# Kernel optimization log

Hardware: AMD Instinct MI355X
Metric: run time of the kernel (lower is better)

## Reference

```python
import jax, jax.numpy as jnp
import numpy as np

TOP_K = 2
SCALING = 32.0 / 16.0  # alpha / rank


def setup_inputs() -> dict:
    key = jax.random.key(0)
    ks = jax.random.split(key, 8)
    B_, S, D = 4, 4096, 2048
    E, R, H = 5, 16, 256
    return {
        "x": jax.random.normal(ks[0], (B_, S, D), jnp.float32),
        "base_output": jax.random.normal(ks[1], (B_, S, D), jnp.float32),
        "A": jax.random.normal(ks[2], (E, D, R), jnp.float32) * (1.0 / R),
        "B": jax.random.normal(ks[3], (E, R, D), jnp.float32) * 0.02,
        "W1": jax.random.normal(ks[4], (D, H), jnp.float32) * (1.0 / np.sqrt(D)),
        "b1": jnp.zeros((H,), jnp.float32),
        "W2": jax.random.normal(ks[5], (H, E), jnp.float32) * (1.0 / np.sqrt(H)),
        "b2": jnp.zeros((E,), jnp.float32),
    }


def reference(x, base_output, A, B, W1, b1, W2, b2):
    # Router: Linear -> SiLU -> Linear -> softmax
    routing_logits = jax.nn.silu(x @ W1 + b1) @ W2 + b2          # [B,S,E]
    routing_weights = jax.nn.softmax(routing_logits, axis=-1)
    top_k_weights, top_k_indices = jax.lax.top_k(routing_weights, TOP_K)  # [B,S,K]
    top_k_weights = top_k_weights / top_k_weights.sum(-1, keepdims=True)

    # Dense per-expert LoRA eval (faithful to original): x @ A_e @ B_e * scaling
    low = jnp.einsum('bsd,edr->bser', x, A)                       # [B,S,E,R]
    expert_outputs = jnp.einsum('bser,erd->bsed', low, B) * SCALING  # [B,S,E,D]

    # Gather selected experts and combine with normalized weights
    gathered = jnp.take_along_axis(expert_outputs, top_k_indices[..., None], axis=2)  # [B,S,K,D]
    combined = (gathered * top_k_weights[..., None]).sum(axis=2)  # [B,S,D]
    return base_output + combined
```

## Files before the change

kernel.cpp:

```cpp
#include <hip/hip_runtime.h>
#include <math.h>

#define N_TOK 16384
#define D_DIM 2048
#define H_DIM 256
#define E_NUM 5
#define R_DIM 16
#define ER 80

#define NCT 21
#define KG_N 64

typedef _Float16 half8 __attribute__((ext_vector_type(8)));
typedef float f32x4 __attribute__((ext_vector_type(4)));

__global__ __launch_bounds__(256) void pack_w_kernel(
    const float* __restrict__ W1, const float* __restrict__ A,
    _Float16* __restrict__ Whi, _Float16* __restrict__ Wlo) {
  const int idx = blockIdx.x * 256 + threadIdx.x;
  const int lane = idx & 63;
  const int kgct = idx >> 6;
  const int kg = kgct & 63;
  const int ct = kgct >> 6;
  const int k0 = kg * 32 + ((lane >> 4) << 3);
  const int par = lane & 15;
  float v[8];
  if (ct < 16) {
    const int col = ct * 16 + par;
#pragma unroll
    for (int j = 0; j < 8; ++j) v[j] = W1[(size_t)(k0 + j) * H_DIM + col];
  } else {
    const float* Ae = A + (size_t)(ct - 16) * D_DIM * R_DIM;
#pragma unroll
    for (int j = 0; j < 8; ++j) v[j] = Ae[(size_t)(k0 + j) * R_DIM + par];
  }
  half8 hv, lv;
#pragma unroll
  for (int j = 0; j < 8; ++j) {
    const _Float16 hh = (_Float16)v[j];
    hv[j] = hh;
    lv[j] = (_Float16)(v[j] - (float)hh);
  }
  ((half8*)Whi)[(size_t)kgct * 64 + lane] = hv;
  ((half8*)Wlo)[(size_t)kgct * 64 + lane] = lv;
}

__global__ __launch_bounds__(256, 3) void xgemm_kernel(
    const float* __restrict__ x, const float* __restrict__ b1,
    const _Float16* __restrict__ Whi, const _Float16* __restrict__ Wlo,
    const float* __restrict__ W2, float* __restrict__ plog,
    float* __restrict__ P) {
  __shared__ _Float16 lds[2][2][4][64][8];
  __shared__ float w2s[H_DIM * E_NUM];
  __shared__ float plbuf[4][64][E_NUM];
  const int t = threadIdx.x;
  const int tok0 = blockIdx.x * 64;
  const int y = blockIdx.y;
  const int lane = t & 63;
  const int w = t >> 6;
  const int sr = t >> 2;
  const int sq = t & 3;
  const int lq = lane >> 4;
  const int lp = lane & 15;

  const float* xrow = x + (size_t)(tok0 + sr) * D_DIM + (sq << 3);

  {
    float xv[8];
    *(float4*)&xv[0] = *(const float4*)(xrow);
    *(float4*)&xv[4] = *(const float4*)(xrow + 4);
    half8 hv, lv;
#pragma unroll
    for (int j = 0; j < 8; ++j) {
      const _Float16 hh = (_Float16)xv[j];
      hv[j] = hh;
      lv[j] = (_Float16)(xv[j] - (float)hh);
    }
    *(half8*)&lds[0][0][sq][sr ^ sq][0] = hv;
    *(half8*)&lds[0][1][sq][sr ^ sq][0] = lv;
  }

  const half8* WH = (const half8*)Whi;
  const half8* WL = (const half8*)Wlo;

  if (y < 2) {
    f32x4 acc[4][2];
#pragma unroll
    for (int i = 0; i < 4; ++i)
#pragma unroll
      for (int j = 0; j < 2; ++j) acc[i][j] = (f32x4)0.f;
    const int ctg0 = (y << 3) + (w << 1);
    int cur = 0;
    for (int kg = 0; kg < KG_N; ++kg) {
      __syncthreads();
      const bool more = (kg < KG_N - 1);
      float xv[8];
      if (more) {
        const float* src = xrow + (kg + 1) * 32;
        *(float4*)&xv[0] = *(const float4*)(src);
        *(float4*)&xv[4] = *(const float4*)(src + 4);
      }
      half8 bh[2], bl[2];
#pragma unroll
      for (int ct = 0; ct < 2; ++ct) {
        const size_t wo = ((size_t)(ctg0 + ct) * 64 + kg) * 64 + lane;
        bh[ct] = WH[wo];
        bl[ct] = WL[wo];
      }
#pragma unroll
      for (int rt = 0; rt < 4; ++rt) {
        const int r = ((rt << 4) + lp) ^ lq;
        const half8 ah = *(const half8*)&lds[cur][0][lq][r][0];
        const half8 al = *(const half8*)&lds[cur][1][lq][r][0];
#pragma unroll
        for (int ct = 0; ct < 2; ++ct) {
          acc[rt][ct] = __builtin_amdgcn_mfma_f32_16x16x32_f16(al, bh[ct], acc[rt][ct], 0, 0, 0);
          acc[rt][ct] = __builtin_amdgcn_mfma_f32_16x16x32_f16(ah, bl[ct], acc[rt][ct], 0, 0, 0);
          acc[rt][ct] = __builtin_amdgcn_mfma_f32_16x16x32_f16(ah, bh[ct], acc[rt][ct], 0, 0, 0);
        }
      }
      if (more) {
        half8 hv, lv;
#pragma unroll
        for (int j = 0; j < 8; ++j) {
          const _Float16 hh = (_Float16)xv[j];
          hv[j] = hh;
          lv[j] = (_Float16)(xv[j] - (float)hh);
        }
        *(half8*)&lds[cur ^ 1][0][sq][sr ^ sq][0] = hv;
        *(half8*)&lds[cur ^ 1][1][sq][sr ^ sq][0] = lv;
      }
      cur ^= 1;
    }

    for (int i = t; i < H_DIM * E_NUM; i += 256) w2s[i] = W2[i];
    __syncthreads();
    const int colb = (y << 7) + (w << 5);
#pragma unroll
    for (int rt = 0; rt < 4; ++rt) {
      float pl[4][5];
#pragma unroll
      for (int rg = 0; rg < 4; ++rg)
#pragma unroll
        for (int e = 0; e < 5; ++e) pl[rg][e] = 0.f;
#pragma unroll
      for (int ct = 0; ct < 2; ++ct) {
        const int col = colb + (ct << 4) + lp;
        const float bb = b1[col];
        float w2c[5];
#pragma unroll
        for (int e = 0; e < 5; ++e) w2c[e] = w2s[col * 5 + e];
#pragma unroll
        for (int rg = 0; rg < 4; ++rg) {
          float v = acc[rt][ct][rg] + bb;
          v = v / (1.f + expf(-v));
#pragma unroll
          for (int e = 0; e < 5; ++e) pl[rg][e] = fmaf(v, w2c[e], pl[rg][e]);
        }
      }
#pragma unroll
      for (int m = 1; m < 16; m <<= 1)
#pragma unroll
        for (int rg = 0; rg < 4; ++rg)
#pragma unroll
          for (int e = 0; e < 5; ++e) pl[rg][e] += __shfl_xor(pl[rg][e], m, 64);
      if (lp == 0) {
        const int rl0 = (rt << 4) + (lq << 2);
#pragma unroll
        for (int rg = 0; rg < 4; ++rg)
#pragma unroll
          for (int e = 0; e < 5; ++e) plbuf[w][rl0 + rg][e] = pl[rg][e];
      }
    }
    __syncthreads();
    for (int i = t; i < 64 * E_NUM; i += 256) {
      const int row = i / E_NUM;
      const int e = i - row * E_NUM;
      const float s = plbuf[0][row][e] + plbuf[1][row][e] +
                      plbuf[2][row][e] + plbuf[3][row][e];
      plog[((size_t)y * N_TOK + tok0 + row) * E_NUM + e] = s;
    }
  } else {
    f32x4 acc[5];
#pragma unroll
    for (int j = 0; j < 5; ++j) acc[j] = (f32x4)0.f;
    int cur = 0;
    for (int kg = 0; kg < KG_N; ++kg) {
      __syncthreads();
      const bool more = (kg < KG_N - 1);
      float xv[8];
      if (more) {
        const float* src = xrow + (kg + 1) * 32;
        *(float4*)&xv[0] = *(const float4*)(src);
        *(float4*)&xv[4] = *(const float4*)(src + 4);
      }
      half8 bh[5], bl[5];
#pragma unroll
      for (int ct = 0; ct < 5; ++ct) {
        const size_t wo = ((size_t)(16 + ct) * 64 + kg) * 64 + lane;
        bh[ct] = WH[wo];
        bl[ct] = WL[wo];
      }
      {
        const int r = ((w << 4) + lp) ^ lq;
        const half8 ah = *(const half8*)&lds[cur][0][lq][r][0];
        const half8 al = *(const half8*)&lds[cur][1][lq][r][0];
#pragma unroll
        for (int ct = 0; ct < 5; ++ct) {
          acc[ct] = __builtin_amdgcn_mfma_f32_16x16x32_f16(al, bh[ct], acc[ct], 0, 0, 0);
          acc[ct] = __builtin_amdgcn_mfma_f32_16x16x32_f16(ah, bl[ct], acc[ct], 0, 0, 0);
          acc[ct] = __builtin_amdgcn_mfma_f32_16x16x32_f16(ah, bh[ct], acc[ct], 0, 0, 0);
        }
      }
      if (more) {
        half8 hv, lv;
#pragma unroll
        for (int j = 0; j < 8; ++j) {
          const _Float16 hh = (_Float16)xv[j];
          hv[j] = hh;
          lv[j] = (_Float16)(xv[j] - (float)hh);
        }
        *(half8*)&lds[cur ^ 1][0][sq][sr ^ sq][0] = hv;
        *(half8*)&lds[cur ^ 1][1][sq][sr ^ sq][0] = lv;
      }
      cur ^= 1;
    }
#pragma unroll
    for (int ct = 0; ct < 5; ++ct)
#pragma unroll
      for (int rg = 0; rg < 4; ++rg) {
        const int row = tok0 + (w << 4) + (lq << 2) + rg;
        P[(size_t)row * ER + (ct << 4) + lp] = acc[ct][rg];
      }
  }
}

__global__ __launch_bounds__(256, 4) void combine_kernel(
    const float* __restrict__ P, const float* __restrict__ Bm,
    const float* __restrict__ base, const float* __restrict__ plog,
    const float* __restrict__ b2, float* __restrict__ out) {
  __shared__ float Pl[32][80];
  __shared__ float sc[32][5];
  const int t = threadIdx.x;
  const int wg = __builtin_amdgcn_readfirstlane(t >> 6);
  const int c4 = ((blockIdx.x & 7) << 8) + ((t & 63) << 2);
  const int tokb = (blockIdx.x >> 3) << 5;
  const int r0 = wg << 3;

  if (t < 32) {
    const float* p0 = plog + (size_t)(tokb + t) * E_NUM;
    const float* p1 = plog + ((size_t)N_TOK + tokb + t) * E_NUM;
    float lg[5];
#pragma unroll
    for (int e = 0; e < 5; ++e) lg[e] = p0[e] + p1[e] + b2[e];
    int e0 = 0;
#pragma unroll
    for (int e = 1; e < 5; ++e) if (lg[e] > lg[e0]) e0 = e;
    int e1 = (e0 == 0) ? 1 : 0;
#pragma unroll
    for (int e = 0; e < 5; ++e) if (e != e0 && lg[e] > lg[e1]) e1 = e;
    const float qq = expf(lg[e1] - lg[e0]);
    const float s0 = 2.f / (1.f + qq);
    const float s1 = qq * s0;
#pragma unroll
    for (int e = 0; e < 5; ++e)
      sc[t][e] = (e == e0) ? s0 : ((e == e1) ? s1 : 0.f);
  }
  __syncthreads();
  for (int idx = t; idx < 640; idx += 256) {
    const int row = idx / 20;
    const int off = (idx % 20) << 2;
    float4 v = *(const float4*)(P + (size_t)(tokb + row) * ER + off);
    v.x *= sc[row][(off + 0) >> 4];
    v.y *= sc[row][(off + 1) >> 4];
    v.z *= sc[row][(off + 2) >> 4];
    v.w *= sc[row][(off + 3) >> 4];
    *(float4*)&Pl[row][off] = v;
  }
  __syncthreads();

  float4 acc[8];
#pragma unroll
  for (int i = 0; i < 8; ++i) acc[i] = make_float4(0.f, 0.f, 0.f, 0.f);

  float4 bmA[4], bmB[4];
#pragma unroll
  for (int r = 0; r < 4; ++r)
    bmA[r] = *(const float4*)(Bm + (size_t)r * D_DIM + c4);

  for (int k0 = 0; k0 < ER; k0 += 8) {
#pragma unroll
    for (int r = 0; r < 4; ++r)
      bmB[r] = *(const float4*)(Bm + (size_t)(k0 + 4 + r) * D_DIM + c4);
#pragma unroll
    for (int i = 0; i < 8; ++i) {
      float pv[4];
      *(float4*)pv = *(const float4*)&Pl[r0 + i][k0];
      acc[i].x = fmaf(pv[0], bmA[0].x, fmaf(pv[1], bmA[1].x, fmaf(pv[2], bmA[2].x, fmaf(pv[3], bmA[3].x, acc[i].x))));
      acc[i].y = fmaf(pv[0], bmA[0].y, fmaf(pv[1], bmA[1].y, fmaf(pv[2], bmA[2].y, fmaf(pv[3], bmA[3].y, acc[i].y))));
      acc[i].z = fmaf(pv[0], bmA[0].z, fmaf(pv[1], bmA[1].z, fmaf(pv[2], bmA[2].z, fmaf(pv[3], bmA[3].z, acc[i].z))));
      acc[i].w = fmaf(pv[0], bmA[0].w, fmaf(pv[1], bmA[1].w, fmaf(pv[2], bmA[2].w, fmaf(pv[3], bmA[3].w, acc[i].w))));
    }
    if (k0 + 8 < ER) {
#pragma unroll
      for (int r = 0; r < 4; ++r)
        bmA[r] = *(const float4*)(Bm + (size_t)(k0 + 8 + r) * D_DIM + c4);
    }
#pragma unroll
    for (int i = 0; i < 8; ++i) {
      float pv[4];
      *(float4*)pv = *(const float4*)&Pl[r0 + i][k0 + 4];
      acc[i].x = fmaf(pv[0], bmB[0].x, fmaf(pv[1], bmB[1].x, fmaf(pv[2], bmB[2].x, fmaf(pv[3], bmB[3].x, acc[i].x))));
      acc[i].y = fmaf(pv[0], bmB[0].y, fmaf(pv[1], bmB[1].y, fmaf(pv[2], bmB[2].y, fmaf(pv[3], bmB[3].y, acc[i].y))));
      acc[i].z = fmaf(pv[0], bmB[0].z, fmaf(pv[1], bmB[1].z, fmaf(pv[2], bmB[2].z, fmaf(pv[3], bmB[3].z, acc[i].z))));
      acc[i].w = fmaf(pv[0], bmB[0].w, fmaf(pv[1], bmB[1].w, fmaf(pv[2], bmB[2].w, fmaf(pv[3], bmB[3].w, acc[i].w))));
    }
  }

#pragma unroll
  for (int i = 0; i < 8; ++i) {
    const size_t o = (size_t)(tokb + r0 + i) * D_DIM + c4;
    const float4 b = *(const float4*)(base + o);
    float4 r;
    r.x = acc[i].x + b.x;
    r.y = acc[i].y + b.y;
    r.z = acc[i].z + b.z;
    r.w = acc[i].w + b.w;
    *(float4*)(out + o) = r;
  }
}

extern "C" void kernel_launch(void* const* d_in, const int* in_sizes, int n_in,
                              void* d_out, int out_size, void* d_ws,
                              size_t ws_size, hipStream_t stream) {
  const float* x  = (const float*)d_in[0];
  const float* bo = (const float*)d_in[1];
  const float* A  = (const float*)d_in[2];
  const float* Bm = (const float*)d_in[3];
  const float* W1 = (const float*)d_in[4];
  const float* b1 = (const float*)d_in[5];
  const float* W2 = (const float*)d_in[6];
  const float* b2 = (const float*)d_in[7];
  float* out = (float*)d_out;

  char* ws = (char*)d_ws;
  float* P = (float*)ws;
  _Float16* Whi = (_Float16*)(ws + 5242880);
  _Float16* Wlo = (_Float16*)(ws + 5242880 + 1376256);
  float* plog = (float*)(ws + 5242880 + 2 * 1376256);

  pack_w_kernel<<<336, 256, 0, stream>>>(W1, A, Whi, Wlo);
  xgemm_kernel<<<dim3(N_TOK / 64, 3), 256, 0, stream>>>(x, b1, Whi, Wlo, W2,
                                                        plog, P);
  combine_kernel<<<(N_TOK / 32) * (D_DIM / 256), 256, 0, stream>>>(
      P, Bm, bo, plog, b2, out);
}
```

Baseline: 442.0 us.

## Use single-fp16 MFMA for LoRA projections and combine, prefetch router weights

The LoRA down-projection in xgemm drops the hi/lo split and runs one fp16 MFMA per tile instead of three. The combine GEMM now uses fp16 MFMA with B pre-packed into fragment layout, replacing the scalar fp32 FMA loop. The router GEMM is unrolled by two so the next k-step's weight fragments are prefetched into registers. The aim is less MFMA and VALU work in the LoRA path and more overlap of weight loads, at the cost of reduced precision in the expert outputs and a scattered scalar store pattern for the output.

Result: faster. 386.5 us (-12.6%).

```diff
diff --git a/kernel.cpp b/kernel.cpp
--- a/kernel.cpp
+++ b/kernel.cpp
@@ -16,34 +16,129 @@
 
 __global__ __launch_bounds__(256) void pack_w_kernel(
     const float* __restrict__ W1, const float* __restrict__ A,
-    _Float16* __restrict__ Whi, _Float16* __restrict__ Wlo) {
+    const float* __restrict__ Bm, _Float16* __restrict__ Whi,
+    _Float16* __restrict__ Wlo, _Float16* __restrict__ Bf) {
   const int idx = blockIdx.x * 256 + threadIdx.x;
   const int lane = idx & 63;
-  const int kgct = idx >> 6;
-  const int kg = kgct & 63;
-  const int ct = kgct >> 6;
-  const int k0 = kg * 32 + ((lane >> 4) << 3);
-  const int par = lane & 15;
-  float v[8];
-  if (ct < 16) {
-    const int col = ct * 16 + par;
-#pragma unroll
-    for (int j = 0; j < 8; ++j) v[j] = W1[(size_t)(k0 + j) * H_DIM + col];
+  if (idx < 86016) {
+    const int kgct = idx >> 6;
+    const int kg = kgct & 63;
+    const int ct = kgct >> 6;
+    const int k0 = kg * 32 + ((lane >> 4) << 3);
+    const int par = lane & 15;
+    float v[8];
+    if (ct < 16) {
+      const int col = ct * 16 + par;
+#pragma unroll
+      for (int j = 0; j < 8; ++j) v[j] = W1[(size_t)(k0 + j) * H_DIM + col];
+    } else {
+      const float* Ae = A + (size_t)(ct - 16) * D_DIM * R_DIM;
+#pragma unroll
+      for (int j = 0; j < 8; ++j) v[j] = Ae[(size_t)(k0 + j) * R_DIM + par];
+    }
+    half8 hv, lv;
+#pragma unroll
+    for (int j = 0; j < 8; ++j) {
+      const _Float16 hh = (_Float16)v[j];
+      hv[j] = hh;
+      lv[j] = (_Float16)(v[j] - (float)hh);
+    }
+    ((half8*)Whi)[(size_t)kgct * 64 + lane] = hv;
+    ((half8*)Wlo)[(size_t)kgct * 64 + lane] = lv;
   } else {
-    const float* Ae = A + (size_t)(ct - 16) * D_DIM * R_DIM;
-#pragma unroll
-    for (int j = 0; j < 8; ++j) v[j] = Ae[(size_t)(k0 + j) * R_DIM + par];
-  }
-  half8 hv, lv;
-#pragma unroll
-  for (int j = 0; j < 8; ++j) {
-    const _Float16 hh = (_Float16)v[j];
-    hv[j] = hh;
-    lv[j] = (_Float16)(v[j] - (float)hh);
-  }
-  ((half8*)Whi)[(size_t)kgct * 64 + lane] = hv;
-  ((half8*)Wlo)[(size_t)kgct * 64 + lane] = lv;
+    const int u = (idx - 86016) >> 6;
+    const int s = u % 3;
+    const int ct = u / 3;
+    const int col = ct * 16 + (lane & 15);
+    const int kb = s * 32 + ((lane >> 4) << 3);
+    half8 hv;
+#pragma unroll
+    for (int j = 0; j < 8; ++j) {
+      const int k = kb + j;
+      hv[j] = (k < ER) ? (_Float16)Bm[(size_t)k * D_DIM + col] : (_Float16)0.f;
+    }
+    ((half8*)Bf)[(size_t)u * 64 + lane] = hv;
+  }
 }
+
+#define W_BODY(USE_H, USE_L, PRE_H, PRE_L, KG)                               \
+  __syncthreads();                                                           \
+  {                                                                          \
+    const int kn = (KG) + 1;                                                 \
+    if (kn < KG_N) {                                                         \
+      _Pragma("unroll") for (int ct = 0; ct < 2; ++ct) {                     \
+        const size_t wo = ((size_t)(ctg0 + ct) * 64 + kn) * 64 + lane;       \
+        PRE_H[ct] = WH[wo];                                                  \
+        PRE_L[ct] = WL[wo];                                                  \
+      }                                                                      \
+    }                                                                        \
+    float xv[8];                                                             \
+    const bool more = (KG) < KG_N - 1;                                       \
+    if (more) {                                                              \
+      const float* src = xrow + ((KG) + 1) * 32;                             \
+      *(float4*)&xv[0] = *(const float4*)(src);                              \
+      *(float4*)&xv[4] = *(const float4*)(src + 4);                          \
+    }                                                                        \
+    _Pragma("unroll") for (int rt = 0; rt < 4; ++rt) {                       \
+      const int r = ((rt << 4) + lp) ^ lq;                                   \
+      const half8 ah = *(const half8*)&lds[cur][0][lq][r][0];                \
+      const half8 al = *(const half8*)&lds[cur][1][lq][r][0];                \
+      _Pragma("unroll") for (int ct = 0; ct < 2; ++ct) {                     \
+        acc[rt][ct] = __builtin_amdgcn_mfma_f32_16x16x32_f16(                \
+            al, USE_H[ct], acc[rt][ct], 0, 0, 0);                            \
+        acc[rt][ct] = __builtin_amdgcn_mfma_f32_16x16x32_f16(                \
+            ah, USE_L[ct], acc[rt][ct], 0, 0, 0);                            \
+        acc[rt][ct] = __builtin_amdgcn_mfma_f32_16x16x32_f16(                \
+            ah, USE_H[ct], acc[rt][ct], 0, 0, 0);                            \
+      }                                                                      \
+    }                                                                        \
+    if (more) {                                                              \
+      half8 hv, lv;                                                          \
+      _Pragma("unroll") for (int j = 0; j < 8; ++j) {                        \
+        const _Float16 hh = (_Float16)xv[j];                                 \
+        hv[j] = hh;                                                          \
+        lv[j] = (_Float16)(xv[j] - (float)hh);                               \
+      }                                                                      \
+      *(half8*)&lds[cur ^ 1][0][sq][sr ^ sq][0] = hv;                        \
+      *(half8*)&lds[cur ^ 1][1][sq][sr ^ sq][0] = lv;                        \
+    }                                                                        \
+    cur ^= 1;                                                                \
+  }
+
+#define P_BODY(USE_H, PRE_H, KG)                                             \
+  __syncthreads();                                                           \
+  {                                                                          \
+    const int kn = (KG) + 1;                                                 \
+    if (kn < KG_N) {                                                         \
+      _Pragma("unroll") for (int ct = 0; ct < 5; ++ct) {                     \
+        const size_t wo = ((size_t)(16 + ct) * 64 + kn) * 64 + lane;         \
+        PRE_H[ct] = WH[wo];                                                  \
+      }                                                                      \
+    }                                                                        \
+    float xv[8];                                                             \
+    const bool more = (KG) < KG_N - 1;                                       \
+    if (more) {                                                              \
+      const float* src = xrow + ((KG) + 1) * 32;                             \
+      *(float4*)&xv[0] = *(const float4*)(src);                              \
+      *(float4*)&xv[4] = *(const float4*)(src + 4);                          \
+    }                                                                        \
+    {                                                                        \
+      const int r = ((w << 4) + lp) ^ lq;                                    \
+      const half8 ah = *(const half8*)&lds[cur][0][lq][r][0];                \
+      _Pragma("unroll") for (int ct = 0; ct < 5; ++ct) {                     \
+        acc[ct] = __builtin_amdgcn_mfma_f32_16x16x32_f16(                    \
+            ah, USE_H[ct], acc[ct], 0, 0, 0);                                \
+      }                                                                      \
+    }                                                                        \
+    if (more) {                                                              \
+      half8 hv;                                                              \
+      _Pragma("unroll") for (int j = 0; j < 8; ++j) {                        \
+        hv[j] = (_Float16)xv[j];                                             \
+      }                                                                      \
+      *(half8*)&lds[cur ^ 1][0][sq][sr ^ sq][0] = hv;                        \
+    }                                                                        \
+    cur ^= 1;                                                                \
+  }
 
 __global__ __launch_bounds__(256, 3) void xgemm_kernel(
     const float* __restrict__ x, const float* __restrict__ b1,
@@ -77,7 +172,7 @@
       lv[j] = (_Float16)(xv[j] - (float)hh);
     }
     *(half8*)&lds[0][0][sq][sr ^ sq][0] = hv;
-    *(half8*)&lds[0][1][sq][sr ^ sq][0] = lv;
+    if (y < 2) *(half8*)&lds[0][1][sq][sr ^ sq][0] = lv;
   }
 
   const half8* WH = (const half8*)Whi;
@@ -90,47 +185,19 @@
 #pragma unroll
       for (int j = 0; j < 2; ++j) acc[i][j] = (f32x4)0.f;
     const int ctg0 = (y << 3) + (w << 1);
+
+    half8 bhA[2], blA[2], bhB[2], blB[2];
+#pragma unroll
+    for (int ct = 0; ct < 2; ++ct) {
+      const size_t wo = ((size_t)(ctg0 + ct) * 64 + 0) * 64 + lane;
+      bhA[ct] = WH[wo];
+      blA[ct] = WL[wo];
+    }
+
     int cur = 0;
-    for (int kg = 0; kg < KG_N; ++kg) {
-      __syncthreads();
-      const bool more = (kg < KG_N - 1);
-      float xv[8];
-      if (more) {
-        const float* src = xrow + (kg + 1) * 32;
-        *(float4*)&xv[0] = *(const float4*)(src);
-        *(float4*)&xv[4] = *(const float4*)(src + 4);
-      }
-      half8 bh[2], bl[2];
-#pragma unroll
-      for (int ct = 0; ct < 2; ++ct) {
-        const size_t wo = ((size_t)(ctg0 + ct) * 64 + kg) * 64 + lane;
-        bh[ct] = WH[wo];
-        bl[ct] = WL[wo];
-      }
-#pragma unroll
-      for (int rt = 0; rt < 4; ++rt) {
-        const int r = ((rt << 4) + lp) ^ lq;
-        const half8 ah = *(const half8*)&lds[cur][0][lq][r][0];
-        const half8 al = *(const half8*)&lds[cur][1][lq][r][0];
-#pragma unroll
-        for (int ct = 0; ct < 2; ++ct) {
-          acc[rt][ct] = __builtin_amdgcn_mfma_f32_16x16x32_f16(al, bh[ct], acc[rt][ct], 0, 0, 0);
-          acc[rt][ct] = __builtin_amdgcn_mfma_f32_16x16x32_f16(ah, bl[ct], acc[rt][ct], 0, 0, 0);
-          acc[rt][ct] = __builtin_amdgcn_mfma_f32_16x16x32_f16(ah, bh[ct], acc[rt][ct], 0, 0, 0);
-        }
-      }
-      if (more) {
-        half8 hv, lv;
-#pragma unroll
-        for (int j = 0; j < 8; ++j) {
-          const _Float16 hh = (_Float16)xv[j];
-          hv[j] = hh;
-          lv[j] = (_Float16)(xv[j] - (float)hh);
-        }
-        *(half8*)&lds[cur ^ 1][0][sq][sr ^ sq][0] = hv;
-        *(half8*)&lds[cur ^ 1][1][sq][sr ^ sq][0] = lv;
-      }
-      cur ^= 1;
+    for (int kg = 0; kg < KG_N; kg += 2) {
+      W_BODY(bhA, blA, bhB, blB, kg)
+      W_BODY(bhB, blB, bhA, blA, kg + 1)
     }
 
     for (int i = t; i < H_DIM * E_NUM; i += 256) w2s[i] = W2[i];
@@ -184,46 +251,18 @@
     f32x4 acc[5];
 #pragma unroll
     for (int j = 0; j < 5; ++j) acc[j] = (f32x4)0.f;
+
+    half8 bhA[5], bhB[5];
+#pragma unroll
+    for (int ct = 0; ct < 5; ++ct) {
+      const size_t wo = ((size_t)(16 + ct) * 64 + 0) * 64 + lane;
+      bhA[ct] = WH[wo];
+    }
+
     int cur = 0;
-    for (int kg = 0; kg < KG_N; ++kg) {
-      __syncthreads();
-      const bool more = (kg < KG_N - 1);
-      float xv[8];
-      if (more) {
-        const float* src = xrow + (kg + 1) * 32;
-        *(float4*)&xv[0] = *(const float4*)(src);
-        *(float4*)&xv[4] = *(const float4*)(src + 4);
-      }
-      half8 bh[5], bl[5];
-#pragma unroll
-      for (int ct = 0; ct < 5; ++ct) {
-        const size_t wo = ((size_t)(16 + ct) * 64 + kg) * 64 + lane;
-        bh[ct] = WH[wo];
-        bl[ct] = WL[wo];
-      }
-      {
-        const int r = ((w << 4) + lp) ^ lq;
-        const half8 ah = *(const half8*)&lds[cur][0][lq][r][0];
-        const half8 al = *(const half8*)&lds[cur][1][lq][r][0];
-#pragma unroll
-        for (int ct = 0; ct < 5; ++ct) {
-          acc[ct] = __builtin_amdgcn_mfma_f32_16x16x32_f16(al, bh[ct], acc[ct], 0, 0, 0);
-          acc[ct] = __builtin_amdgcn_mfma_f32_16x16x32_f16(ah, bl[ct], acc[ct], 0, 0, 0);
-          acc[ct] = __builtin_amdgcn_mfma_f32_16x16x32_f16(ah, bh[ct], acc[ct], 0, 0, 0);
-        }
-      }
-      if (more) {
-        half8 hv, lv;
-#pragma unroll
-        for (int j = 0; j < 8; ++j) {
-          const _Float16 hh = (_Float16)xv[j];
-          hv[j] = hh;
-          lv[j] = (_Float16)(xv[j] - (float)hh);
-        }
-        *(half8*)&lds[cur ^ 1][0][sq][sr ^ sq][0] = hv;
-        *(half8*)&lds[cur ^ 1][1][sq][sr ^ sq][0] = lv;
-      }
-      cur ^= 1;
+    for (int kg = 0; kg < KG_N; kg += 2) {
+      P_BODY(bhA, bhB, kg)
+      P_BODY(bhB, bhA, kg + 1)
     }
 #pragma unroll
     for (int ct = 0; ct < 5; ++ct)
@@ -235,17 +274,46 @@
   }
 }
 
-__global__ __launch_bounds__(256, 4) void combine_kernel(
-    const float* __restrict__ P, const float* __restrict__ Bm,
+__global__ __launch_bounds__(256, 2) void combine_kernel(
+    const float* __restrict__ P, const _Float16* __restrict__ Bf,
     const float* __restrict__ base, const float* __restrict__ plog,
     const float* __restrict__ b2, float* __restrict__ out) {
-  __shared__ float Pl[32][80];
+  __shared__ _Float16 Pl[32][104];
   __shared__ float sc[32][5];
   const int t = threadIdx.x;
-  const int wg = __builtin_amdgcn_readfirstlane(t >> 6);
-  const int c4 = ((blockIdx.x & 7) << 8) + ((t & 63) << 2);
-  const int tokb = (blockIdx.x >> 3) << 5;
-  const int r0 = wg << 3;
+  const int lane = t & 63;
+  const int w = t >> 6;
+  const int bx = blockIdx.x;
+  const int tokb = (bx >> 3) << 5;
+  const int colb = (bx & 7) << 8;
+  const int lp = lane & 15;
+  const int lq = lane >> 4;
+
+  const int u0r = t / 12, u0c = (t % 12) << 3;
+  float4 pa0 = make_float4(0.f, 0.f, 0.f, 0.f), pb0 = pa0;
+  if (u0c < ER) {
+    const float* pr = P + (size_t)(tokb + u0r) * ER + u0c;
+    pa0 = *(const float4*)pr;
+    pb0 = *(const float4*)(pr + 4);
+  }
+  const int u1 = t + 256;
+  const int u1r = u1 / 12, u1c = (u1 % 12) << 3;
+  const bool has1 = (t < 128);
+  float4 pa1 = make_float4(0.f, 0.f, 0.f, 0.f), pb1 = pa1;
+  if (has1 && u1c < ER) {
+    const float* pr = P + (size_t)(tokb + u1r) * ER + u1c;
+    pa1 = *(const float4*)pr;
+    pb1 = *(const float4*)(pr + 4);
+  }
+
+  const half8* BH = (const half8*)Bf;
+  const int ctg = (colb >> 4) + (w << 2);
+  half8 bf[4][3];
+#pragma unroll
+  for (int ct = 0; ct < 4; ++ct)
+#pragma unroll
+    for (int s = 0; s < 3; ++s)
+      bf[ct][s] = BH[(size_t)((ctg + ct) * 3 + s) * 64 + lane];
 
   if (t < 32) {
     const float* p0 = plog + (size_t)(tokb + t) * E_NUM;
@@ -267,67 +335,55 @@
       sc[t][e] = (e == e0) ? s0 : ((e == e1) ? s1 : 0.f);
   }
   __syncthreads();
-  for (int idx = t; idx < 640; idx += 256) {
-    const int row = idx / 20;
-    const int off = (idx % 20) << 2;
-    float4 v = *(const float4*)(P + (size_t)(tokb + row) * ER + off);
-    v.x *= sc[row][(off + 0) >> 4];
-    v.y *= sc[row][(off + 1) >> 4];
-    v.z *= sc[row][(off + 2) >> 4];
-    v.w *= sc[row][(off + 3) >> 4];
-    *(float4*)&Pl[row][off] = v;
+  {
+    const float s0 = (u0c < ER) ? sc[u0r][u0c >> 4] : 0.f;
+    half8 hv;
+    hv[0] = (_Float16)(pa0.x * s0); hv[1] = (_Float16)(pa0.y * s0);
+    hv[2] = (_Float16)(pa0.z * s0); hv[3] = (_Float16)(pa0.w * s0);
+    hv[4] = (_Float16)(pb0.x * s0); hv[5] = (_Float16)(pb0.y * s0);
+    hv[6] = (_Float16)(pb0.z * s0); hv[7] = (_Float16)(pb0.w * s0);
+    *(half8*)&Pl[u0r][u0c] = hv;
+    if (has1) {
+      const float s1v = (u1c < ER) ? sc[u1r][u1c >> 4] : 0.f;
+      half8 h2;
+      h2[0] = (_Float16)(pa1.x * s1v); h2[1] = (_Float16)(pa1.y * s1v);
+      h2[2] = (_Float16)(pa1.z * s1v); h2[3] = (_Float16)(pa1.w * s1v);
+      h2[4] = (_Float16)(pb1.x * s1v); h2[5] = (_Float16)(pb1.y * s1v);
+      h2[6] = (_Float16)(pb1.z * s1v); h2[7] = (_Float16)(pb1.w * s1v);
+      *(half8*)&Pl[u1r][u1c] = h2;
+    }
   }
   __syncthreads();
 
-  float4 acc[8];
-#pragma unroll
-  for (int i = 0; i < 8; ++i) acc[i] = make_float4(0.f, 0.f, 0.f, 0.f);
-
-  float4 bmA[4], bmB[4];
-#pragma unroll
-  for (int r = 0; r < 4; ++r)
-    bmA[r] = *(const float4*)(Bm + (size_t)r * D_DIM + c4);
-
-  for (int k0 = 0; k0 < ER; k0 += 8) {
-#pragma unroll
-    for (int r = 0; r < 4; ++r)
-      bmB[r] = *(const float4*)(Bm + (size_t)(k0 + 4 + r) * D_DIM + c4);
-#pragma unroll
-    for (int i = 0; i < 8; ++i) {
-      float pv[4];
-      *(float4*)pv = *(const float4*)&Pl[r0 + i][k0];
-      acc[i].x = fmaf(pv[0], bmA[0].x, fmaf(pv[1], bmA[1].x, fmaf(pv[2], bmA[2].x, fmaf(pv[3], bmA[3].x, acc[i].x))));
-      acc[i].y = fmaf(pv[0], bmA[0].y, fmaf(pv[1], bmA[1].y, fmaf(pv[2], bmA[2].y, fmaf(pv[3], bmA[3].y, acc[i].y))));
-      acc[i].z = fmaf(pv[0], bmA[0].z, fmaf(pv[1], bmA[1].z, fmaf(pv[2], bmA[2].z, fmaf(pv[3], bmA[3].z, acc[i].z))));
-      acc[i].w = fmaf(pv[0], bmA[0].w, fmaf(pv[1], bmA[1].w, fmaf(pv[2], bmA[2].w, fmaf(pv[3], bmA[3].w, acc[i].w))));
-    }
-    if (k0 + 8 < ER) {
-#pragma unroll
-      for (int r = 0; r < 4; ++r)
-        bmA[r] = *(const float4*)(Bm + (size_t)(k0 + 8 + r) * D_DIM + c4);
-    }
-#pragma unroll
-    for (int i = 0; i < 8; ++i) {
-      float pv[4];
-      *(float4*)pv = *(const float4*)&Pl[r0 + i][k0 + 4];
-      acc[i].x = fmaf(pv[0], bmB[0].x, fmaf(pv[1], bmB[1].x, fmaf(pv[2], bmB[2].x, fmaf(pv[3], bmB[3].x, acc[i].x))));
-      acc[i].y = fmaf(pv[0], bmB[0].y, fmaf(pv[1], bmB[1].y, fmaf(pv[2], bmB[2].y, fmaf(pv[3], bmB[3].y, acc[i].y))));
-      acc[i].z = fmaf(pv[0], bmB[0].z, fmaf(pv[1], bmB[1].z, fmaf(pv[2], bmB[2].z, fmaf(pv[3], bmB[3].z, acc[i].z))));
-      acc[i].w = fmaf(pv[0], bmB[0].w, fmaf(pv[1], bmB[1].w, fmaf(pv[2], bmB[2].w, fmaf(pv[3], bmB[3].w, acc[i].w))));
-    }
-  }
-
-#pragma unroll
-  for (int i = 0; i < 8; ++i) {
-    const size_t o = (size_t)(tokb + r0 + i) * D_DIM + c4;
-    const float4 b = *(const float4*)(base + o);
-    float4 r;
-    r.x = acc[i].x + b.x;
-    r.y = acc[i].y + b.y;
-    r.z = acc[i].z + b.z;
-    r.w = acc[i].w + b.w;
-    *(float4*)(out + o) = r;
-  }
+  f32x4 acc[2][4];
+#pragma unroll
+  for (int rt = 0; rt < 2; ++rt)
+#pragma unroll
+    for (int ct = 0; ct < 4; ++ct) acc[rt][ct] = (f32x4)0.f;
+
+#pragma unroll
+  for (int rt = 0; rt < 2; ++rt)
+#pragma unroll
+    for (int s = 0; s < 3; ++s) {
+      const half8 a = *(const half8*)&Pl[(rt << 4) + lp][(s << 5) + (lq << 3)];
+#pragma unroll
+      for (int ct = 0; ct < 4; ++ct)
+        acc[rt][ct] = __builtin_amdgcn_mfma_f32_16x16x32_f16(
+            a, bf[ct][s], acc[rt][ct], 0, 0, 0);
+    }
+
+#pragma unroll
+  for (int rt = 0; rt < 2; ++rt)
+#pragma unroll
+    for (int ct = 0; ct < 4; ++ct) {
+      const int col = colb + (w << 6) + (ct << 4) + lp;
+#pragma unroll
+      for (int rg = 0; rg < 4; ++rg) {
+        const int row = tokb + (rt << 4) + (lq << 2) + rg;
+        const size_t o = (size_t)row * D_DIM + col;
+        out[o] = acc[rt][ct][rg] + base[o];
+      }
+    }
 }
 
 extern "C" void kernel_launch(void* const* d_in, const int* in_sizes, int n_in,
@@ -348,10 +404,11 @@
   _Float16* Whi = (_Float16*)(ws + 5242880);
   _Float16* Wlo = (_Float16*)(ws + 5242880 + 1376256);
   float* plog = (float*)(ws + 5242880 + 2 * 1376256);
-
-  pack_w_kernel<<<336, 256, 0, stream>>>(W1, A, Whi, Wlo);
+  _Float16* Bf = (_Float16*)(ws + 5242880 + 2 * 1376256 + 655360);
+
+  pack_w_kernel<<<432, 256, 0, stream>>>(W1, A, Bm, Whi, Wlo, Bf);
   xgemm_kernel<<<dim3(N_TOK / 64, 3), 256, 0, stream>>>(x, b1, Whi, Wlo, W2,
                                                         plog, P);
   combine_kernel<<<(N_TOK / 32) * (D_DIM / 256), 256, 0, stream>>>(
-      P, Bm, bo, plog, b2, out);
+      P, Bf, bo, plog, b2, out);
 }
```
